# Optimization experiments

Measured on AMD Instinct MI355X. Metric: run time of the kernel, lower is better.

## Reference

```python
import jax, jax.numpy as jnp
import numpy as np

BATCH = 4096
IN_F = 1024
OUT_F = 1024
GRID_SIZE = 8
SPLINE_ORDER = 3
SCALE_SPLINE = 1.0


def setup_inputs() -> dict:
    key = jax.random.key(0)
    kx, kb, ks = jax.random.split(key, 3)
    # inputs live on the spline domain [-1, 1]
    x = jax.random.uniform(kx, (BATCH, IN_F), jnp.float32, -1.0, 1.0)
    # kaiming_uniform_(a=sqrt(5)) on (out,in) -> U(-1/sqrt(in), 1/sqrt(in))
    bound = 1.0 / float(np.sqrt(IN_F))
    base_weight = jax.random.uniform(kb, (OUT_F, IN_F), jnp.float32, -bound, bound)
    # normal(mean=0, std=0.1), (out, in, grid_size + spline_order)
    spline_weight = 0.1 * jax.random.normal(ks, (OUT_F, IN_F, GRID_SIZE + SPLINE_ORDER), jnp.float32)
    # uniform knot vector with spacing h = 2/grid_size over [-1,1], extended by
    # spline_order knots on each side so Cox-de Boor yields grid_size+spline_order bases
    h = 2.0 / GRID_SIZE
    grid = jnp.arange(-SPLINE_ORDER, GRID_SIZE + SPLINE_ORDER + 1, dtype=jnp.float32) * h - 1.0
    return {"x": x, "base_weight": base_weight, "spline_weight": spline_weight, "grid": grid}


def b_spline_basis(x, grid, k):
    # x: (batch, in), grid: (grid_size + 2k + 1,) shared across (out, in) pairs
    xe = x[..., None]  # (b, i, 1)
    # degree-0: indicator of knot interval -> (b, i, grid_size + 2k)
    basis = ((xe >= grid[:-1]) & (xe < grid[1:])).astype(x.dtype)
    for d in range(1, k + 1):  # Cox-de Boor recursion up to degree k
        left_denom = grid[d:-1] - grid[:-(d + 1)]
        right_denom = grid[d + 1:] - grid[1:-d]
        left_denom = jnp.where(left_denom > 0, left_denom, 1.0)
        right_denom = jnp.where(right_denom > 0, right_denom, 1.0)
        basis = ((xe - grid[:-(d + 1)]) / left_denom * basis[..., :-1]
                 + (grid[d + 1:] - xe) / right_denom * basis[..., 1:])
    return basis  # (b, i, grid_size + k)


def reference(x, base_weight, spline_weight, grid):
    base_output = x @ base_weight.T  # (b, out)
    basis = b_spline_basis(x, grid, SPLINE_ORDER)  # (b, i, L), L = grid_size + k
    # grid is identical for every (out, in) pair, so the per-(o,i) basis of the
    # original collapses to a per-i basis; einsum 'bil,oil->bo' is the same math.
    spline_output = jnp.einsum('bil,oil->bo', basis, spline_weight)
    return base_output + SCALE_SPLINE * spline_output
```

## Files before the change

kernel.cpp:

```cpp
#include <hip/hip_runtime.h>
#include <hip/hip_bf16.h>
#include <cstdint>

#define BATCH 4096
#define INF   1024
#define OUTF  1024
#define LCH   12
#define KTOT  (INF*LCH)
#define BM    256
#define BN    256
#define BK    48
#define NT    64
#define THREADS 512
#define TSZ   (6*256*8)

#define WTT_BYTES ((size_t)OUTF * KTOT * 2)
#define PART_FLOATS ((size_t)BATCH * OUTF)
#define OUT_BYTES (PART_FLOATS * 4)

typedef __bf16 bf16x8 __attribute__((ext_vector_type(8)));
typedef float  f32x16 __attribute__((ext_vector_type(16)));
typedef unsigned long long ull;
typedef unsigned short us;

struct alignas(16) U2 { ull x, y; };

__device__ __forceinline__ us f2bf(float f) {
  unsigned int u = __builtin_bit_cast(unsigned int, f);
  u += 0x7FFFu + ((u >> 16) & 1u);
  return (us)(u >> 16);
}

__device__ __forceinline__ void async_copy16(const void* g, void* l) {
  __builtin_amdgcn_global_load_lds(
      (const __attribute__((address_space(1))) unsigned int*)g,
      (__attribute__((address_space(3))) unsigned int*)l,
      16, 0, 0);
}

#define PIPE_BARRIER() do {                                        \
  asm volatile("s_waitcnt vmcnt(4) lgkmcnt(0)" ::: "memory");      \
  __builtin_amdgcn_sched_barrier(0);                               \
  __builtin_amdgcn_s_barrier();                                    \
  __builtin_amdgcn_sched_barrier(0);                               \
} while (0)

__device__ __forceinline__ void basis12(float xx, ull W[3]) {
  float u  = fmaf(xx, 4.0f, 7.0f);
  float fm = floorf(u);
  int   mi = (int)fm;
  float t  = u - fm;
  float s  = 1.0f - t;
  float t2 = t * t, t3 = t2 * t;
  float w0 = (s * s * s) * (1.0f / 6.0f);
  float w3 = t3 * (1.0f / 6.0f);
  float w1 = fmaf(0.5f, t3, 2.0f / 3.0f) - t2;
  float w2 = 1.0f - w0 - w1 - w3;
  int ls = mi - 3;
  ull W64 = (ull)f2bf(w0)
          | ((ull)f2bf(w1) << 16)
          | ((ull)f2bf(w2) << 32)
          | ((ull)f2bf(w3) << 48);
  int sh = ls << 4;
  int a  = sh & 63;
  ull lop  = W64 << a;
  ull hip_ = a ? (W64 >> (64 - a)) : 0ull;
  W[0] = (sh < 64) ? lop : 0ull;
  W[1] = (sh < 64) ? hip_ : lop;
  W[2] = ((sh < 64) ? 0ull : hip_) | ((ull)f2bf(xx) << 48);
}

__global__ __launch_bounds__(256) void kan_build_wtT(
    const float* __restrict__ sw,
    const float* __restrict__ bw,
    us* __restrict__ WtT)
{
  int t   = blockIdx.x * 256 + threadIdx.x;
  int col = t & 255;
  int q   = t >> 8;
  int fp  = q & 1;
  int ktG = (q >> 1) & 255;
  int bn  = q >> 9;
  int o   = bn * 256 + col;
  int i0  = ktG * 4 + fp * 2;

  us v[24];
#pragma unroll
  for (int j = 0; j < 2; ++j) {
    int i = i0 + j;
    const float* s = sw + (size_t)(o * 1024 + i) * 11;
#pragma unroll
    for (int l = 0; l < 11; ++l) v[j * 12 + l] = f2bf(s[l]);
    v[j * 12 + 11] = f2bf(bw[o * 1024 + i]);
  }
  int g0 = fp * 3;
  us* base = WtT + (size_t)(bn * 256 + ktG) * (6 * 256 * 8);
  U2* p = reinterpret_cast<U2*>(base);
#pragma unroll
  for (int j = 0; j < 3; ++j) {
    U2 u;
    const us* w = v + j * 8;
    u.x = (ull)w[0] | ((ull)w[1] << 16) | ((ull)w[2] << 32) | ((ull)w[3] << 48);
    u.y = (ull)w[4] | ((ull)w[5] << 16) | ((ull)w[6] << 32) | ((ull)w[7] << 48);
    p[(g0 + j) * 256 + col] = u;
  }
}

#define BASIS2(XV, W0_,W1_,W2_,W3_,W4_,W5_) do {                         \
  {                                                                      \
    float xx = (XV).x;                                                   \
    float u_  = fmaf(xx, 4.0f, 7.0f);                                    \
    float fm_ = floorf(u_);                                              \
    int   mi_ = (int)fm_;                                                \
    float t_  = u_ - fm_;                                                \
    float s_  = 1.0f - t_;                                               \
    float t2_ = t_ * t_, t3_ = t2_ * t_;                                 \
    float w0_ = (s_ * s_ * s_) * (1.0f / 6.0f);                          \
    float w3_ = t3_ * (1.0f / 6.0f);                                     \
    float w1_ = fmaf(0.5f, t3_, 2.0f / 3.0f) - t2_;                      \
    float w2_ = 1.0f - w0_ - w1_ - w3_;                                  \
    unsigned int p01_, p23_;                                             \
    asm("v_cvt_pk_bf16_f32 %0, %1, %2" : "=v"(p01_) : "v"(w0_), "v"(w1_)); \
    asm("v_cvt_pk_bf16_f32 %0, %1, %2" : "=v"(p23_) : "v"(w2_), "v"(w3_)); \
    ull W64_ = (ull)p01_ | ((ull)p23_ << 32);                            \
    int sh_ = (mi_ - 3) << 4;                                            \
    int a_  = sh_ & 63;                                                  \
    ull lo_ = W64_ << a_;                                                \
    ull hi_ = a_ ? (W64_ >> (64 - a_)) : 0ull;                           \
    W0_ = (sh_ < 64) ? lo_ : 0ull;                                       \
    W1_ = (sh_ < 64) ? hi_ : lo_;                                        \
    W2_ = ((sh_ < 64) ? 0ull : hi_) | ((ull)f2bf(xx) << 48);             \
  }                                                                      \
  {                                                                      \
    float xx = (XV).y;                                                   \
    float u_  = fmaf(xx, 4.0f, 7.0f);                                    \
    float fm_ = floorf(u_);                                              \
    int   mi_ = (int)fm_;                                                \
    float t_  = u_ - fm_;                                                \
    float s_  = 1.0f - t_;                                               \
    float t2_ = t_ * t_, t3_ = t2_ * t_;                                 \
    float w0_ = (s_ * s_ * s_) * (1.0f / 6.0f);                          \
    float w3_ = t3_ * (1.0f / 6.0f);                                     \
    float w1_ = fmaf(0.5f, t3_, 2.0f / 3.0f) - t2_;                      \
    float w2_ = 1.0f - w0_ - w1_ - w3_;                                  \
    unsigned int p01_, p23_;                                             \
    asm("v_cvt_pk_bf16_f32 %0, %1, %2" : "=v"(p01_) : "v"(w0_), "v"(w1_)); \
    asm("v_cvt_pk_bf16_f32 %0, %1, %2" : "=v"(p23_) : "v"(w2_), "v"(w3_)); \
    ull W64_ = (ull)p01_ | ((ull)p23_ << 32);                            \
    int sh_ = (mi_ - 3) << 4;                                            \
    int a_  = sh_ & 63;                                                  \
    ull lo_ = W64_ << a_;                                                \
    ull hi_ = a_ ? (W64_ >> (64 - a_)) : 0ull;                           \
    W3_ = (sh_ < 64) ? lo_ : 0ull;                                       \
    W4_ = (sh_ < 64) ? hi_ : lo_;                                        \
    W5_ = ((sh_ < 64) ? 0ull : hi_) | ((ull)f2bf(xx) << 48);             \
  }                                                                      \
} while (0)

__global__ __launch_bounds__(THREADS, 2) void kan_gemm(
    const float* __restrict__ x,
    const us* __restrict__ WtT,
    float* __restrict__ P)
{
  __shared__ alignas(16) us smem[5 * TSZ];

  const int tid  = threadIdx.x;
  const int lane = tid & 63;
  const int wid  = tid >> 6;
  const int wm   = (wid >> 2) * 128;
  const int wn   = (wid & 3) * 64;
  const int lo   = lane & 31;
  const int lh   = lane >> 5;
  const int b    = (int)blockIdx.x;
  const int bn   = b & 3;
  const int kq   = (b >> 2) & 3;
  const int bm   = b >> 4;

  const int r   = tid & 255;
  const int fp  = tid >> 8;
  const int g0A = fp * 3;
  const float* xrow = x + (size_t)(bm * BM + r) * INF + kq * 256 + fp * 2;

  us* Acur = smem;
  us* Aalt = smem + TSZ;
  us* Bcur = smem + 2 * TSZ;
  us* Bnxt = smem + 3 * TSZ;
  us* Bnn  = smem + 4 * TSZ;

  f32x16 acc[4][2] = {};

  auto stageB = [&](int c, us* Bd) {
    const int ktG = kq * NT + c;
    const us* base = WtT + (size_t)(bn * 256 + ktG) * (6 * 256 * 8);
#pragma unroll
    for (int j = 0; j < 3; ++j) {
      int s = wid * 3 + j;
      int g = s >> 2, h = s & 3;
      async_copy16(base + g * 2048 + h * 512 + lane * 8,
                   Bd + g * 2048 + h * 512);
    }
  };

#define WRITEW(AD, W0_,W1_,W2_,W3_,W4_,W5_) do {                   \
    U2* p_ = reinterpret_cast<U2*>(AD);                            \
    U2 u0_; u0_.x = W0_; u0_.y = W1_;                              \
    U2 u1_; u1_.x = W2_; u1_.y = W3_;                              \
    U2 u2_; u2_.x = W4_; u2_.y = W5_;                              \
    p_[(g0A + 0) * 256 + r] = u0_;                                 \
    p_[(g0A + 1) * 256 + r] = u1_;                                 \
    p_[(g0A + 2) * 256 + r] = u2_;                                 \
  } while (0)

#define READK(S, A0,A1,A2,A3,B0,B1) do {                           \
    const int kk_ = (S) * 2 + lh;                                  \
    A0 = *reinterpret_cast<const bf16x8*>(&Acur[(kk_ * 256 + wm +  0 + lo) * 8]); \
    A1 = *reinterpret_cast<const bf16x8*>(&Acur[(kk_ * 256 + wm + 32 + lo) * 8]); \
    A2 = *reinterpret_cast<const bf16x8*>(&Acur[(kk_ * 256 + wm + 64 + lo) * 8]); \
    A3 = *reinterpret_cast<const bf16x8*>(&Acur[(kk_ * 256 + wm + 96 + lo) * 8]); \
    B0 = *reinterpret_cast<const bf16x8*>(&Bcur[(kk_ * 256 + wn +  0 + lo) * 8]); \
    B1 = *reinterpret_cast<const bf16x8*>(&Bcur[(kk_ * 256 + wn + 32 + lo) * 8]); \
  } while (0)

#define MFMAK(A0,A1,A2,A3,B0,B1) do {                              \
    acc[0][0] = __builtin_amdgcn_mfma_f32_32x32x16_bf16(A0, B0, acc[0][0], 0, 0, 0); \
    acc[0][1] = __builtin_amdgcn_mfma_f32_32x32x16_bf16(A0, B1, acc[0][1], 0, 0, 0); \
    acc[1][0] = __builtin_amdgcn_mfma_f32_32x32x16_bf16(A1, B0, acc[1][0], 0, 0, 0); \
    acc[1][1] = __builtin_amdgcn_mfma_f32_32x32x16_bf16(A1, B1, acc[1][1], 0, 0, 0); \
    acc[2][0] = __builtin_amdgcn_mfma_f32_32x32x16_bf16(A2, B0, acc[2][0], 0, 0, 0); \
    acc[2][1] = __builtin_amdgcn_mfma_f32_32x32x16_bf16(A2, B1, acc[2][1], 0, 0, 0); \
    acc[3][0] = __builtin_amdgcn_mfma_f32_32x32x16_bf16(A3, B0, acc[3][0], 0, 0, 0); \
    acc[3][1] = __builtin_amdgcn_mfma_f32_32x32x16_bf16(A3, B1, acc[3][1], 0, 0, 0); \
  } while (0)

  {
    float2 x0 = *reinterpret_cast<const float2*>(xrow);
    ull W0, W1, W2, W3, W4, W5;
    BASIS2(x0, W0, W1, W2, W3, W4, W5);
    WRITEW(Acur, W0, W1, W2, W3, W4, W5);
    stageB(0, Bcur);
    stageB(1, Bnxt);
  }
  float2 xa = *reinterpret_cast<const float2*>(xrow + 4);
  PIPE_BARRIER();

  for (int c = 0; c < NT; ++c) {
    const int cf = (c + 2 < NT) ? (c + 2) : (NT - 1);

    float2 xb = *reinterpret_cast<const float2*>(xrow + cf * 4);
    stageB(cf, Bnn);

    ull W0, W1, W2, W3, W4, W5;
    bf16x8 a00, a01, a02, a03, b00, b01;
    bf16x8 a10, a11, a12, a13, b10, b11;
    bf16x8 a20, a21, a22, a23, b20, b21;

    READK(0, a00, a01, a02, a03, b00, b01);
    BASIS2(xa, W0, W1, W2, W3, W4, W5);
    READK(1, a10, a11, a12, a13, b10, b11);
    MFMAK(a00, a01, a02, a03, b00, b01);
    READK(2, a20, a21, a22, a23, b20, b21);
    MFMAK(a10, a11, a12, a13, b10, b11);
    __builtin_amdgcn_sched_barrier(0);
    WRITEW(Aalt, W0, W1, W2, W3, W4, W5);
    MFMAK(a20, a21, a22, a23, b20, b21);

    PIPE_BARRIER();

    us* t = Bcur; Bcur = Bnxt; Bnxt = Bnn; Bnn = t;
    t = Acur; Acur = Aalt; Aalt = t;
    xa = xb;
  }

  asm volatile("s_waitcnt vmcnt(0) lgkmcnt(0)" ::: "memory");

  float* dst = P + (size_t)kq * PART_FLOATS;
#pragma unroll
  for (int f = 0; f < 4; ++f) {
#pragma unroll
    for (int rr = 0; rr < 16; ++rr) {
      int row = bm * BM + wm + f * 32 + (rr & 3) + 8 * (rr >> 2) + 4 * lh;
      float* orow = dst + (size_t)row * OUTF + bn * BN + wn + lo;
#pragma unroll
      for (int n = 0; n < 2; ++n)
        orow[n * 32] = acc[f][n][rr];
    }
  }
}

__global__ __launch_bounds__(256) void kan_reduce4(
    float4* __restrict__ out, const float4* __restrict__ p)
{
  size_t i = (size_t)blockIdx.x * 256 + threadIdx.x;
  const size_t Q = PART_FLOATS / 4;
  float4 a = p[i], bq = p[i + Q], c = p[i + 2 * Q], d = p[i + 3 * Q];
  float4 o;
  o.x = (a.x + bq.x) + (c.x + d.x);
  o.y = (a.y + bq.y) + (c.y + d.y);
  o.z = (a.z + bq.z) + (c.z + d.z);
  o.w = (a.w + bq.w) + (c.w + d.w);
  out[i] = o;
}

#define FB_BUFSZ (6*128*8)

__global__ __launch_bounds__(256) void kan_build_wt(
    const float* __restrict__ sw, const float* __restrict__ bw,
    us* __restrict__ Wt)
{
  int idx = blockIdx.x * 256 + threadIdx.x;
  int o = idx >> 10;
  int i = idx & 1023;
  const float* s = sw + (size_t)(o * 1024 + i) * 11;
  us v[12];
#pragma unroll
  for (int l = 0; l < 11; ++l) v[l] = f2bf(s[l]);
  v[11] = f2bf(bw[o * 1024 + i]);
  us* d = Wt + (size_t)o * KTOT + i * 12;
  *reinterpret_cast<ushort4*>(d + 0) = make_ushort4(v[0], v[1], v[2],  v[3]);
  *reinterpret_cast<ushort4*>(d + 4) = make_ushort4(v[4], v[5], v[6],  v[7]);
  *reinterpret_cast<ushort4*>(d + 8) = make_ushort4(v[8], v[9], v[10], v[11]);
}

__global__ __launch_bounds__(512, 4) void kan_gemm_fb(
    const float* __restrict__ x, const us* __restrict__ Wt,
    float* __restrict__ out)
{
  __shared__ alignas(16) us smem[5 * FB_BUFSZ];
  const int tid  = threadIdx.x;
  const int lane = tid & 63;
  const int wid  = tid >> 6;
  const int wm   = (wid >> 2) * 64;
  const int wn   = (wid & 3) * 32;
  const int lo   = lane & 31;
  const int lh   = lane >> 5;
  const int idx  = (int)blockIdx.x;
  const int bn   = idx & 7;
  const int kh   = (idx >> 3) & 1;
  const int bm   = idx >> 4;
  const bool builder = (tid < 256);
  const bool stager  = (wid >= 4);
  const int ab  = tid & 127;
  const int ai0 = ((tid >> 7) & 1) << 1;
  const float* xrow = x + (size_t)(bm * 128 + ab) * INF + kh * 512 + ai0;
  const size_t kbase = (size_t)kh * (KTOT / 2);

  us* Bcur = smem;            us* Bnxt = smem + FB_BUFSZ;
  us* Bnn  = smem + 2 * FB_BUFSZ;
  us* Acur = smem + 3 * FB_BUFSZ; us* Aalt = smem + 4 * FB_BUFSZ;
  f32x16 acc[2] = {};

  auto stageB = [&](int c, us* Bd) {
    const int wq = wid - 4;
#pragma unroll
    for (int qq = 0; qq < 3; ++qq) {
      int G  = (wq * 3 + qq) * 64 + lane;
      int kk = G >> 7;
      int oo = G & 127;
      const us* src = Wt + (size_t)(bn * 128 + oo) * KTOT + kbase + c * 48 + kk * 8;
      async_copy16(src, Bd + (wq * 3 + qq) * 512);
    }
  };
  auto buildA = [&](float2 xv, us* Ad) {
    ull W[6];
    basis12(xv.x, W + 0);
    basis12(xv.y, W + 3);
    U2* p = reinterpret_cast<U2*>(Ad);
    const int g0 = (ai0 >> 1) * 3;
    U2 u0; u0.x = W[0]; u0.y = W[1];
    U2 u1; u1.x = W[2]; u1.y = W[3];
    U2 u2; u2.x = W[4]; u2.y = W[5];
    p[(g0 + 0) * 128 + ab] = u0;
    p[(g0 + 1) * 128 + ab] = u1;
    p[(g0 + 2) * 128 + ab] = u2;
  };

  float2 xa = make_float2(0.f, 0.f);
  if (builder) {
    float2 x0v = *reinterpret_cast<const float2*>(xrow);
    buildA(x0v, Acur);
    xa = *reinterpret_cast<const float2*>(xrow + 4);
  }
  if (stager) { stageB(0, Bcur); stageB(1, Bnxt); }
  asm volatile("s_waitcnt vmcnt(3) lgkmcnt(0)" ::: "memory");
  __builtin_amdgcn_s_barrier();

  for (int c = 0; c < 128; ++c) {
    int cf = (c + 2 < 128) ? (c + 2) : 127;
    float2 xb = xa;
    if (builder) {
      xb = *reinterpret_cast<const float2*>(xrow + cf * 4);
      buildA(xa, Aalt);
    }
    if (stager) stageB(cf, Bnn);
#pragma unroll
    for (int s = 0; s < 3; ++s) {
      const int kk = s * 2 + lh;
      bf16x8 a0 = *reinterpret_cast<const bf16x8*>(&Acur[(kk * 128 + wm + lo) * 8]);
      bf16x8 a1 = *reinterpret_cast<const bf16x8*>(&Acur[(kk * 128 + wm + 32 + lo) * 8]);
      bf16x8 b0 = *reinterpret_cast<const bf16x8*>(&Bcur[(kk * 128 + wn + lo) * 8]);
      acc[0] = __builtin_amdgcn_mfma_f32_32x32x16_bf16(a0, b0, acc[0], 0, 0, 0);
      acc[1] = __builtin_amdgcn_mfma_f32_32x32x16_bf16(a1, b0, acc[1], 0, 0, 0);
    }
    asm volatile("s_waitcnt vmcnt(3) lgkmcnt(0)" ::: "memory");
    __builtin_amdgcn_s_barrier();
    us* t = Bcur; Bcur = Bnxt; Bnxt = Bnn; Bnn = t;
    t = Acur; Acur = Aalt; Aalt = t;
    xa = xb;
  }
  asm volatile("s_waitcnt vmcnt(0) lgkmcnt(0)" ::: "memory");
#pragma unroll
  for (int mf = 0; mf < 2; ++mf)
#pragma unroll
    for (int r2 = 0; r2 < 16; ++r2) {
      int row = bm * 128 + wm + mf * 32 + (r2 & 3) + 8 * (r2 >> 2) + 4 * lh;
      atomicAdd(out + (size_t)row * OUTF + bn * 128 + wn + lo, acc[mf][r2]);
    }
}

extern "C" void kernel_launch(void* const* d_in, const int* in_sizes, int n_in,
                              void* d_out, int out_size, void* d_ws, size_t ws_size,
                              hipStream_t stream) {
  const float* x  = (const float*)d_in[0];
  const float* bw = (const float*)d_in[1];
  const float* sw = (const float*)d_in[2];
  float* out = (float*)d_out;

  if (ws_size >= WTT_BYTES + 4 * OUT_BYTES) {
    us* WtT  = (us*)d_ws;
    float* P = (float*)((char*)d_ws + WTT_BYTES);
    kan_build_wtT<<<2048, 256, 0, stream>>>(sw, bw, WtT);
    kan_gemm<<<256, THREADS, 0, stream>>>(x, WtT, P);
    kan_reduce4<<<(int)(PART_FLOATS / 4 / 256), 256, 0, stream>>>(
        (float4*)out, (const float4*)P);
  } else if (ws_size >= WTT_BYTES) {
    us* Wt = (us*)d_ws;
    kan_build_wt<<<(OUTF * INF) / 256, 256, 0, stream>>>(sw, bw, Wt);
    hipMemsetAsync(d_out, 0, OUT_BYTES, stream);
    kan_gemm_fb<<<512, 512, 0, stream>>>(x, Wt, out);
  }
}
```

Measured before the change: 160.8 us.

## Store split-K partials as packed bf16 and vectorize weight-build loads

The GEMM now packs each pair of fp32 split-K partial accumulators into bf16 and writes them as 32-bit words. A new reduce kernel unpacks the four partials, sums them in fp32, and scatters the results back to the correct output columns. This halves the partial-buffer traffic on both the write and the read. The weight-build kernel also loads spline and base weights as float2 instead of scalar floats. The cost is precision: each partial is rounded to bf16 before the final sum, which adds error to the output.

```diff
diff --git a/kernel.cpp b/kernel.cpp
--- a/kernel.cpp
+++ b/kernel.cpp
@@ -16,6 +16,8 @@
 
 #define WTT_BYTES ((size_t)OUTF * KTOT * 2)
 #define PART_FLOATS ((size_t)BATCH * OUTF)
+#define PQ_U32   (PART_FLOATS / 2)
+#define P_BYTES  ((size_t)4 * PQ_U32 * 4)
 #define OUT_BYTES (PART_FLOATS * 4)
 
 typedef __bf16 bf16x8 __attribute__((ext_vector_type(8)));
@@ -84,15 +86,26 @@
   int o   = bn * 256 + col;
   int i0  = ktG * 4 + fp * 2;
 
+  const float2* s2 = reinterpret_cast<const float2*>(
+      sw + (size_t)(o * 1024 + i0) * 11);
+  float2 sv[11];
+#pragma unroll
+  for (int l = 0; l < 11; ++l) sv[l] = s2[l];
+  float2 bv = *reinterpret_cast<const float2*>(bw + (size_t)o * 1024 + i0);
+
   us v[24];
 #pragma unroll
-  for (int j = 0; j < 2; ++j) {
-    int i = i0 + j;
-    const float* s = sw + (size_t)(o * 1024 + i) * 11;
-#pragma unroll
-    for (int l = 0; l < 11; ++l) v[j * 12 + l] = f2bf(s[l]);
-    v[j * 12 + 11] = f2bf(bw[o * 1024 + i]);
-  }
+  for (int l = 0; l < 11; ++l) {
+    int m0 = l;
+    int m1 = 11 + l;
+    float f0 = (m0 & 1) ? sv[m0 >> 1].y : sv[m0 >> 1].x;
+    float f1 = (m1 & 1) ? sv[m1 >> 1].y : sv[m1 >> 1].x;
+    v[l]      = f2bf(f0);
+    v[12 + l] = f2bf(f1);
+  }
+  v[11] = f2bf(bv.x);
+  v[23] = f2bf(bv.y);
+
   int g0 = fp * 3;
   us* base = WtT + (size_t)(bn * 256 + ktG) * (6 * 256 * 8);
   U2* p = reinterpret_cast<U2*>(base);
@@ -160,7 +173,7 @@
 __global__ __launch_bounds__(THREADS, 2) void kan_gemm(
     const float* __restrict__ x,
     const us* __restrict__ WtT,
-    float* __restrict__ P)
+    unsigned int* __restrict__ P)
 {
   __shared__ alignas(16) us smem[5 * TSZ];
 
@@ -273,32 +286,60 @@
 
   asm volatile("s_waitcnt vmcnt(0) lgkmcnt(0)" ::: "memory");
 
-  float* dst = P + (size_t)kq * PART_FLOATS;
+  unsigned int* dst = P + (size_t)kq * PQ_U32;
+  const int ubase = bn * 128 + (wn >> 1) + lo;
 #pragma unroll
   for (int f = 0; f < 4; ++f) {
 #pragma unroll
     for (int rr = 0; rr < 16; ++rr) {
       int row = bm * BM + wm + f * 32 + (rr & 3) + 8 * (rr >> 2) + 4 * lh;
-      float* orow = dst + (size_t)row * OUTF + bn * BN + wn + lo;
-#pragma unroll
-      for (int n = 0; n < 2; ++n)
-        orow[n * 32] = acc[f][n][rr];
-    }
-  }
-}
-
-__global__ __launch_bounds__(256) void kan_reduce4(
-    float4* __restrict__ out, const float4* __restrict__ p)
+      unsigned int pk;
+      asm("v_cvt_pk_bf16_f32 %0, %1, %2"
+          : "=v"(pk) : "v"(acc[f][0][rr]), "v"(acc[f][1][rr]));
+      dst[(size_t)row * 512 + ubase] = pk;
+    }
+  }
+}
+
+__global__ __launch_bounds__(256) void kan_reduce4p(
+    float* __restrict__ out, const uint4* __restrict__ P)
 {
   size_t i = (size_t)blockIdx.x * 256 + threadIdx.x;
-  const size_t Q = PART_FLOATS / 4;
-  float4 a = p[i], bq = p[i + Q], c = p[i + 2 * Q], d = p[i + 3 * Q];
-  float4 o;
-  o.x = (a.x + bq.x) + (c.x + d.x);
-  o.y = (a.y + bq.y) + (c.y + d.y);
-  o.z = (a.z + bq.z) + (c.z + d.z);
-  o.w = (a.w + bq.w) + (c.w + d.w);
-  out[i] = o;
+  const size_t Q = PQ_U32 / 4;
+  uint4 a = P[i], b = P[i + Q], c = P[i + 2 * Q], d = P[i + 3 * Q];
+
+  size_t u0  = i * 4;
+  size_t row = u0 >> 9;
+  int ur  = (int)(u0 & 511);
+  int pq  = ur >> 7;
+  int sub = (ur >> 5) & 3;
+  int lo0 = ur & 31;
+  int col0 = pq * 256 + sub * 64 + lo0;
+
+  float4 vlo, vhi;
+  {
+    unsigned int ua[4] = {a.x, a.y, a.z, a.w};
+    unsigned int ub[4] = {b.x, b.y, b.z, b.w};
+    unsigned int uc[4] = {c.x, c.y, c.z, c.w};
+    unsigned int ud[4] = {d.x, d.y, d.z, d.w};
+    float* plo = &vlo.x;
+    float* phi = &vhi.x;
+#pragma unroll
+    for (int j = 0; j < 4; ++j) {
+      float la = __builtin_bit_cast(float, ua[j] << 16);
+      float lb = __builtin_bit_cast(float, ub[j] << 16);
+      float lc = __builtin_bit_cast(float, uc[j] << 16);
+      float ld = __builtin_bit_cast(float, ud[j] << 16);
+      float ha = __builtin_bit_cast(float, ua[j] & 0xffff0000u);
+      float hb = __builtin_bit_cast(float, ub[j] & 0xffff0000u);
+      float hc = __builtin_bit_cast(float, uc[j] & 0xffff0000u);
+      float hd = __builtin_bit_cast(float, ud[j] & 0xffff0000u);
+      plo[j] = (la + lb) + (lc + ld);
+      phi[j] = (ha + hb) + (hc + hd);
+    }
+  }
+  *reinterpret_cast<float4*>(out + row * 1024 + col0)      = vlo;
+  *reinterpret_cast<float4*>(out + row * 1024 + col0 + 32) = vhi;
 }
 
 #define FB_BUFSZ (6*128*8)
@@ -425,13 +466,13 @@
   const float* sw = (const float*)d_in[2];
   float* out = (float*)d_out;
 
-  if (ws_size >= WTT_BYTES + 4 * OUT_BYTES) {
-    us* WtT  = (us*)d_ws;
-    float* P = (float*)((char*)d_ws + WTT_BYTES);
+  if (ws_size >= WTT_BYTES + P_BYTES) {
+    us* WtT = (us*)d_ws;
+    unsigned int* P = (unsigned int*)((char*)d_ws + WTT_BYTES);
     kan_build_wtT<<<2048, 256, 0, stream>>>(sw, bw, WtT);
     kan_gemm<<<256, THREADS, 0, stream>>>(x, WtT, P);
-    kan_reduce4<<<(int)(PART_FLOATS / 4 / 256), 256, 0, stream>>>(
-        (float4*)out, (const float4*)P);
+    kan_reduce4p<<<(int)(PQ_U32 / 4 / 256), 256, 0, stream>>>(
+        out, (const uint4*)P);
   } else if (ws_size >= WTT_BYTES) {
     us* Wt = (us*)d_ws;
     kan_build_wt<<<(OUTF * INF) / 256, 256, 0, stream>>>(sw, bw, Wt);
```

After: 146.6 us. 8.8% less time.
